# Optimization experiments

Measured on AMD Instinct MI355X. Metric: run time of the kernel, lower is better.

## Reference

```python
import jax, jax.numpy as jnp
import numpy as np

EMBED_DIM = 512
NUM_HEADS = 16
WINDOW = 8
SHIFT = 4
NUM_PATCHES = 64
NEG_INF = -1e9


def _attention_mask():
    # group map over the full patch grid, as in calculate_attention_mask
    P, s, ws = NUM_PATCHES, SHIFT, WINDOW
    g = np.zeros((P, P), dtype=np.float32)
    g[:, -s:] = 1
    g[-s:, :] = 2
    g[-s:, -s:] = 3
    nw = P // ws
    # (h ws a, w ws b) -> (h*w, ws*ws)
    gw = g.reshape(nw, ws, nw, ws).transpose(0, 2, 1, 3).reshape(nw * nw, ws * ws)
    same = gw[:, None, :] == gw[:, :, None]  # column - row == 0 -> allowed
    return jnp.asarray(same)  # (nW, S, S) bool, True = keep


def setup_inputs() -> dict:
    key = jax.random.key(0)
    ks = jax.random.split(key, 5)
    B, P, C = 16, NUM_PATCHES, EMBED_DIM
    sd = 1.0 / np.sqrt(C)
    return {
        "x": jax.random.normal(ks[0], (B, P, P, C), dtype=jnp.float32),
        "w_qkv": jax.random.normal(ks[1], (3 * C, C), dtype=jnp.float32) * sd,
        "b_qkv": jax.random.normal(ks[2], (3 * C,), dtype=jnp.float32) * 0.02,
        "w_out": jax.random.normal(ks[3], (C, C), dtype=jnp.float32) * sd,
        "b_out": jax.random.normal(ks[4], (C,), dtype=jnp.float32) * 0.02,
    }


def reference(x, w_qkv, b_qkv, w_out, b_out):
    B, P, _, C = x.shape
    ws, H = WINDOW, NUM_HEADS
    d = C // H
    nw = P // ws
    S = ws * ws
    scale = d ** (-0.5)

    # shift (roll backwards)
    xs = jnp.roll(x, (-SHIFT, -SHIFT), axis=(1, 2))
    # window partition: (B, nw, ws, nw, ws, C) -> (B*nw*nw, S, C)
    xw = xs.reshape(B, nw, ws, nw, ws, C).transpose(0, 1, 3, 2, 4, 5)
    xw = xw.reshape(B * nw * nw, S, C)

    qkv = xw @ w_qkv.T + b_qkv  # (Bn, S, 3C)
    q, k, v = jnp.split(qkv, 3, axis=-1)
    # head partition: (Bn, S, H, d) -> (Bn, H, S, d)
    part = lambda t: t.reshape(-1, S, H, d).transpose(0, 2, 1, 3)
    q, k, v = part(q), part(k), part(v)

    scores = jnp.einsum('bhqd,bhkd->bhqk', q, k) * scale  # (Bn, H, S, S)

    mask = _attention_mask()  # (nW, S, S) bool
    scores = scores.reshape(B, nw * nw, H, S, S)
    scores = jnp.where(mask[None, :, None], scores, NEG_INF)
    attn = jax.nn.softmax(scores, axis=-1)  # dropout p=0 (inference)
    attn = attn.reshape(B * nw * nw, H, S, S)

    out = jnp.einsum('bhqk,bhkd->bhqd', attn, v)  # (Bn, H, S, d)
    out = out.transpose(0, 2, 1, 3).reshape(B * nw * nw, S, C)  # merge heads
    out = out @ w_out.T + b_out

    # window merge: (B*nw*nw, S, C) -> (B, P, P, C)
    out = out.reshape(B, nw, nw, ws, ws, C).transpose(0, 1, 3, 2, 4, 5)
    out = out.reshape(B, P, P, C)
    # roll forwards
    return jnp.roll(out, (SHIFT, SHIFT), axis=(1, 2))
```

## Files before the change

### kernel.cpp

```cpp
#include <hip/hip_runtime.h>


using f16   = _Float16;
using f16x8 = __attribute__((ext_vector_type(8))) _Float16;
using f16x4 = __attribute__((ext_vector_type(4))) _Float16;
using f32x4 = __attribute__((ext_vector_type(4))) float;

#define MFMA16(a, b, c) __builtin_amdgcn_mfma_f32_16x16x32_f16((a), (b), (c), 0, 0, 0)
#define SCHEDBAR() __builtin_amdgcn_sched_barrier(0)
#define VMCNT0() asm volatile("s_waitcnt vmcnt(0)" ::: "memory")
#define LGKM0()  asm volatile("s_waitcnt lgkmcnt(0)" ::: "memory")
#define BAR()    __builtin_amdgcn_s_barrier()

static constexpr int QK_HALF = 65536 * 512;

__device__ __forceinline__ void nts4f(f32x4 v, float* p) {
  __builtin_nontemporal_store(v, (f32x4*)p);
}

__device__ __forceinline__ int tok2patch(int t) {
  int b = t >> 12, rem = t & 4095;
  int widx = rem >> 6, s = rem & 63;
  int pr = (((widx >> 3) << 3) + (s >> 3) + 4) & 63;
  int pc = (((widx & 7) << 3) + (s & 7) + 4) & 63;
  return ((b << 12) | (pr << 6) | pc) << 9;
}

__device__ __forceinline__ f16x8 cvt8(float4 a, float4 b) {
  f16x8 h = { (f16)a.x, (f16)a.y, (f16)a.z, (f16)a.w,
              (f16)b.x, (f16)b.y, (f16)b.z, (f16)b.w };
  return h;
}

__global__ __launch_bounds__(512, 2) void k_qkv(const float* __restrict__ x,
                                                const float* __restrict__ wq,
                                                const float* __restrict__ bq,
                                                f16* __restrict__ qk,
                                                f16* __restrict__ vt) {
  __shared__ __align__(16) char smem[86016];
  f16* const B0 = (f16*)smem;
  f16* const B1 = (f16*)(smem + 8192);

  const int tid = threadIdx.x;
  const int lane = tid & 63, wave = tid >> 6;
  const int jlo = lane & 15, g = lane >> 4;
  const int bm = blockIdx.x;

  const int nl = tid >> 2, kq = tid & 3;
  const int bslot = (kq ^ ((nl >> 1) & 3)) * 8;

  const int r0 = tok2patch(bm * 256 + wave * 32 + jlo);
  const int r1 = tok2patch(bm * 256 + wave * 32 + 16 + jlo);
  f16x8 af[2][16];
#pragma unroll
  for (int kg = 0; kg < 4; ++kg) {
    float4 t0[4][2], t1[4][2];
#pragma unroll
    for (int k4 = 0; k4 < 4; ++k4) {
      const int ko = (kg * 4 + k4) * 32 + g * 8;
      t0[k4][0] = *(const float4*)(x + r0 + ko);
      t0[k4][1] = *(const float4*)(x + r0 + ko + 4);
      t1[k4][0] = *(const float4*)(x + r1 + ko);
      t1[k4][1] = *(const float4*)(x + r1 + ko + 4);
    }
#pragma unroll
    for (int k4 = 0; k4 < 4; ++k4) {
      af[0][kg * 4 + k4] = cvt8(t0[k4][0], t0[k4][1]);
      af[1][kg * 4 + k4] = cvt8(t1[k4][0], t1[k4][1]);
    }
    SCHEDBAR();
  }

  f32x4 acc[2][8] = {};
  float4 rb[2];
#define LOADB(U2)                                                         \
  do {                                                                    \
    const int bn2_ = (U2) >> 4, k2_ = ((U2) & 15) * 32;                   \
    const float* bs_ = wq + (bn2_ * 128 + nl) * 512 + k2_ + kq * 8;       \
    rb[0] = *(const float4*)(bs_); rb[1] = *(const float4*)(bs_ + 4);     \
  } while (0)
#define WRITEB(Bp) do { *(f16x8*)((Bp) + nl * 32 + bslot) = cvt8(rb[0], rb[1]); } while (0)

  LOADB(0);
  SCHEDBAR();
  VMCNT0();
  WRITEB(B0);
  LOADB(1);
  LGKM0();
  BAR();

#pragma unroll 1
  for (int bn = 0; bn < 12; ++bn) {
    f16* const Cw = (f16*)(smem + 16384 + wave * 8704);
#pragma unroll
    for (int ks = 0; ks < 16; ++ks) {
      const int u = bn * 16 + ks;
      f16* const Bc = (u & 1) ? B1 : B0;
      f16* const Bn = (u & 1) ? B0 : B1;
      f16x8 bf[8];
#pragma unroll
      for (int nt = 0; nt < 8; ++nt) {
        const int n = nt * 16 + jlo;
        bf[nt] = *(const f16x8*)(Bc + n * 32 + ((g ^ ((n >> 1) & 3)) * 8));
      }
      __builtin_amdgcn_s_setprio(1);
#pragma unroll
      for (int mt = 0; mt < 2; ++mt)
#pragma unroll
        for (int nt = 0; nt < 8; ++nt)
          acc[mt][nt] = MFMA16(af[mt][ks], bf[nt], acc[mt][nt]);
      __builtin_amdgcn_s_setprio(0);
      VMCNT0();
      if (u + 1 < 192) WRITEB(Bn);
      SCHEDBAR();
      if (u + 2 < 192) LOADB(u + 2);
      LGKM0();
      BAR();
    }
    float bias[8];
#pragma unroll
    for (int nt = 0; nt < 8; ++nt) bias[nt] = bq[bn * 128 + nt * 16 + jlo];
    if (bn < 8) {
#pragma unroll
      for (int mt = 0; mt < 2; ++mt)
#pragma unroll
        for (int nt = 0; nt < 8; ++nt)
#pragma unroll
          for (int r = 0; r < 4; ++r)
            Cw[(mt * 16 + g * 4 + r) * 136 + nt * 16 + jlo] =
                (f16)(acc[mt][nt][r] + bias[nt]);
      LGKM0();
      f16* const gb = (bn < 4) ? (qk + bn * 128) : (qk + QK_HALF + (bn - 4) * 128);
#pragma unroll
      for (int p = 0; p < 8; ++p) {
        const int lr = (p >> 1) * 8 + (lane >> 3);
        const int ch = (p & 1) * 8 + (lane & 7);
        const int trow = bm * 256 + wave * 32 + lr;
        *(f16x8*)(gb + trow * 512 + ch * 8) = *(const f16x8*)(Cw + lr * 136 + ch * 8);
      }
    } else {
      const int w = (bm * 256 + wave * 32) >> 6;
      const int s0 = (wave * 32) & 63;
#pragma unroll
      for (int hf = 0; hf < 2; ++hf) {
#pragma unroll
        for (int n2 = 0; n2 < 4; ++n2) {
          const int nt = hf * 4 + n2;
#pragma unroll
          for (int mt = 0; mt < 2; ++mt) {
            f16x4 pk = { (f16)(acc[mt][nt][0] + bias[nt]), (f16)(acc[mt][nt][1] + bias[nt]),
                         (f16)(acc[mt][nt][2] + bias[nt]), (f16)(acc[mt][nt][3] + bias[nt]) };
            *(f16x4*)(Cw + (n2 * 16 + jlo) * 48 + mt * 16 + g * 4) = pk;
          }
        }
        LGKM0();
#pragma unroll
        for (int p = 0; p < 4; ++p) {
          const int cl = p * 16 + (lane >> 2);
          const int ch = lane & 3;
          const int n = (bn - 8) * 128 + hf * 64 + cl;
          const int h = n >> 5, d = n & 31;
          *(f16x8*)(vt + ((w * 16 + h) * 32 + d) * 64 + s0 + ch * 8) =
              *(const f16x8*)(Cw + cl * 48 + ch * 8);
        }
      }
    }
#pragma unroll
    for (int mt = 0; mt < 2; ++mt)
#pragma unroll
      for (int nt = 0; nt < 8; ++nt)
        acc[mt][nt] = (f32x4){0.f, 0.f, 0.f, 0.f};
  }
#undef LOADB
#undef WRITEB
}

__global__ __launch_bounds__(256) void k_attn(const f16* __restrict__ qk,
                                              const f16* __restrict__ vt,
                                              f16* __restrict__ ao) {
  __shared__ f16 P[4][64 * 72];
  const int w = blockIdx.x;
  const int widx = w & 63;
  const bool er = (widx >> 3) == 7;
  const bool ec = (widx & 7) == 7;
  const int tid = threadIdx.x;
  const int lane = tid & 63, wave = tid >> 6;
  const int jlo = lane & 15, g = lane >> 4;
  const int tb = w * 64;
  f16* Pw = P[wave];
  const float scale = 0.17677669529663687f;

#pragma unroll 1
  for (int hh = 0; hh < 4; ++hh) {
    const int h = wave * 4 + hh;
    f16x8 qa[4], kb[4];
#pragma unroll
    for (int mt = 0; mt < 4; ++mt)
      qa[mt] = *(const f16x8*)(qk + (tb + mt * 16 + jlo) * 512 + h * 32 + g * 8);
#pragma unroll
    for (int nt = 0; nt < 4; ++nt)
      kb[nt] = *(const f16x8*)(qk + QK_HALF + (tb + nt * 16 + jlo) * 512 + h * 32 + g * 8);
    f32x4 sc[4][4] = {};
#pragma unroll
    for (int mt = 0; mt < 4; ++mt)
#pragma unroll
      for (int nt = 0; nt < 4; ++nt)
        sc[mt][nt] = MFMA16(qa[mt], kb[nt], sc[mt][nt]);

    int gj[4];
#pragma unroll
    for (int nt = 0; nt < 4; ++nt) {
      int j = nt * 16 + jlo;
      gj[nt] = ((er && ((j >> 3) >= 4)) ? 2 : 0) | ((ec && ((j & 7) >= 4)) ? 1 : 0);
    }
    float rinv[4][4];
#pragma unroll
    for (int mt = 0; mt < 4; ++mt) {
#pragma unroll
      for (int r = 0; r < 4; ++r) {
        const int i = mt * 16 + g * 4 + r;
        const int gi = ((er && ((i >> 3) >= 4)) ? 2 : 0) | ((ec && ((i & 7) >= 4)) ? 1 : 0);
        float v0 = (gi == gj[0]) ? sc[mt][0][r] * scale : -1e9f;
        float v1 = (gi == gj[1]) ? sc[mt][1][r] * scale : -1e9f;
        float v2 = (gi == gj[2]) ? sc[mt][2][r] * scale : -1e9f;
        float v3 = (gi == gj[3]) ? sc[mt][3][r] * scale : -1e9f;
        float m = fmaxf(fmaxf(v0, v1), fmaxf(v2, v3));
        m = fmaxf(m, __shfl_xor(m, 1));
        m = fmaxf(m, __shfl_xor(m, 2));
        m = fmaxf(m, __shfl_xor(m, 4));
        m = fmaxf(m, __shfl_xor(m, 8));
        float p0 = __expf(v0 - m), p1 = __expf(v1 - m);
        float p2 = __expf(v2 - m), p3 = __expf(v3 - m);
        float s = p0 + p1 + p2 + p3;
        s += __shfl_xor(s, 1);
        s += __shfl_xor(s, 2);
        s += __shfl_xor(s, 4);
        s += __shfl_xor(s, 8);
        rinv[mt][r] = 1.0f / s;
        sc[mt][0][r] = p0; sc[mt][1][r] = p1; sc[mt][2][r] = p2; sc[mt][3][r] = p3;
      }
    }
#pragma unroll
    for (int mt = 0; mt < 4; ++mt)
#pragma unroll
      for (int nt = 0; nt < 4; ++nt)
#pragma unroll
        for (int r = 0; r < 4; ++r)
          Pw[(mt * 16 + g * 4 + r) * 72 + nt * 16 + jlo] = (f16)sc[mt][nt][r];
    asm volatile("s_waitcnt lgkmcnt(0)" ::: "memory");

    f32x4 o[4][2] = {};
#pragma unroll
    for (int ks = 0; ks < 2; ++ks) {
      f16x8 pa[4], vb[2];
#pragma unroll
      for (int mt = 0; mt < 4; ++mt)
        pa[mt] = *(const f16x8*)((const char*)Pw + (mt * 16 + jlo) * 144 + ks * 64 + g * 16);
#pragma unroll
      for (int nt = 0; nt < 2; ++nt)
        vb[nt] = *(const f16x8*)(vt + ((w * 16 + h) * 32 + nt * 16 + jlo) * 64 + ks * 32 + g * 8);
#pragma unroll
      for (int mt = 0; mt < 4; ++mt)
#pragma unroll
        for (int nt = 0; nt < 2; ++nt)
          o[mt][nt] = MFMA16(pa[mt], vb[nt], o[mt][nt]);
    }
#pragma unroll
    for (int mt = 0; mt < 4; ++mt)
#pragma unroll
      for (int nt = 0; nt < 2; ++nt)
#pragma unroll
        for (int r = 0; r < 4; ++r)
          Pw[(mt * 16 + g * 4 + r) * 40 + nt * 16 + jlo] =
              (f16)(o[mt][nt][r] * rinv[mt][r]);
    f16* arow = ao + (tb + lane) * 512 + h * 32;
#pragma unroll
    for (int c = 0; c < 4; ++c)
      *(f16x8*)(arow + c * 8) = *(const f16x8*)(Pw + lane * 40 + c * 8);
  }
}

__global__ __launch_bounds__(512, 2) void k_out(const f16* __restrict__ ao,
                                                const float* __restrict__ wo,
                                                const float* __restrict__ bo,
                                                float* __restrict__ out) {
  __shared__ __align__(16) char smem[86016];
  f16* const B0 = (f16*)smem;
  f16* const B1 = (f16*)(smem + 8192);

  const int tid = threadIdx.x;
  const int lane = tid & 63, wave = tid >> 6;
  const int jlo = lane & 15, g = lane >> 4;
  const int bm = blockIdx.x;

  const int nl = tid >> 2, kq = tid & 3;
  const int bslot = (kq ^ ((nl >> 1) & 3)) * 8;

  const f16* const a0 = ao + (bm * 256 + wave * 32 + jlo) * 512 + g * 8;
  const f16* const a1 = a0 + 16 * 512;
  f16x8 af[2][16];
#pragma unroll
  for (int ks = 0; ks < 16; ++ks) {
    af[0][ks] = *(const f16x8*)(a0 + ks * 32);
    af[1][ks] = *(const f16x8*)(a1 + ks * 32);
  }

  f32x4 acc[2][8] = {};
  float4 rb[2];
#define LOADB(U2)                                                         \
  do {                                                                    \
    const int bn2_ = (U2) >> 4, k2_ = ((U2) & 15) * 32;                   \
    const float* bs_ = wo + (bn2_ * 128 + nl) * 512 + k2_ + kq * 8;       \
    rb[0] = *(const float4*)(bs_); rb[1] = *(const float4*)(bs_ + 4);     \
  } while (0)
#define WRITEB(Bp) do { *(f16x8*)((Bp) + nl * 32 + bslot) = cvt8(rb[0], rb[1]); } while (0)

  LOADB(0);
  SCHEDBAR();
  VMCNT0();
  WRITEB(B0);
  LOADB(1);
  LGKM0();
  BAR();

#pragma unroll 1
  for (int bn = 0; bn < 4; ++bn) {
    float* const Cw = (float*)(smem + 16384 + wave * 8704);
#pragma unroll
    for (int ks = 0; ks < 16; ++ks) {
      const int u = bn * 16 + ks;
      f16* const Bc = (u & 1) ? B1 : B0;
      f16* const Bn = (u & 1) ? B0 : B1;
      f16x8 bf[8];
#pragma unroll
      for (int nt = 0; nt < 8; ++nt) {
        const int n = nt * 16 + jlo;
        bf[nt] = *(const f16x8*)(Bc + n * 32 + ((g ^ ((n >> 1) & 3)) * 8));
      }
      __builtin_amdgcn_s_setprio(1);
#pragma unroll
      for (int mt = 0; mt < 2; ++mt)
#pragma unroll
        for (int nt = 0; nt < 8; ++nt)
          acc[mt][nt] = MFMA16(af[mt][ks], bf[nt], acc[mt][nt]);
      __builtin_amdgcn_s_setprio(0);
      VMCNT0();
      if (u + 1 < 64) WRITEB(Bn);
      SCHEDBAR();
      if (u + 2 < 64) LOADB(u + 2);
      LGKM0();
      BAR();
    }
#pragma unroll
    for (int hf = 0; hf < 2; ++hf) {
#pragma unroll
      for (int n2 = 0; n2 < 4; ++n2) {
        const int nt = hf * 4 + n2;
        const float bias = bo[bn * 128 + nt * 16 + jlo];
#pragma unroll
        for (int mt = 0; mt < 2; ++mt)
#pragma unroll
          for (int r = 0; r < 4; ++r)
            Cw[(mt * 16 + g * 4 + r) * 68 + n2 * 16 + jlo] = acc[mt][nt][r] + bias;
      }
      LGKM0();
#pragma unroll
      for (int p = 0; p < 8; ++p) {
        const int lr = (p >> 1) * 8 + (lane >> 3);
        const int ch = (p & 1) * 8 + (lane & 7);
        const int trow = bm * 256 + wave * 32 + lr;
        nts4f(*(const f32x4*)(Cw + lr * 68 + ch * 4),
              out + tok2patch(trow) + bn * 128 + hf * 64 + ch * 4);
      }
      LGKM0();
    }
#pragma unroll
    for (int mt = 0; mt < 2; ++mt)
#pragma unroll
      for (int nt = 0; nt < 8; ++nt)
        acc[mt][nt] = (f32x4){0.f, 0.f, 0.f, 0.f};
  }
#undef LOADB
#undef WRITEB
}

extern "C" void kernel_launch(void* const* d_in, const int* in_sizes, int n_in,
                              void* d_out, int out_size, void* d_ws, size_t ws_size,
                              hipStream_t stream) {
  const float* x  = (const float*)d_in[0];
  const float* wq = (const float*)d_in[1];
  const float* bq = (const float*)d_in[2];
  const float* wo = (const float*)d_in[3];
  const float* bo = (const float*)d_in[4];
  float* out = (float*)d_out;

  f16* qk = (f16*)d_out;
  f16* ao = (f16*)d_ws;
  f16* vt = (f16*)((char*)d_ws + (64u << 20));

  k_qkv<<<dim3(256), 512, 0, stream>>>(x, wq, bq, qk, vt);
  k_attn<<<dim3(1024), 256, 0, stream>>>(qk, vt, ao);
  k_out<<<dim3(256), 512, 0, stream>>>(ao, wo, bo, out);
}
```

Measured before the change: 377.4 us.

## Process two k-steps per barrier with quad-buffered weight tiles in GEMM kernels

In both the QKV and output-projection GEMM kernels, the main loop now consumes two 32-wide k-slices per iteration, using four LDS B buffers and two register staging sets. This halves the number of block barriers and LDS-wait points per tile. The epilogue is folded into the flattened loop, and its scratch area moves to make room for the extra buffers. The trade-off is a larger LDS footprint and a runtime k-index into the A-fragment register array, which may force dynamic register indexing or scratch spills.

Result: slower. 420.7 us (+11.4%).

```diff
diff --git a/kernel.cpp b/kernel.cpp
--- a/kernel.cpp
+++ b/kernel.cpp
@@ -37,17 +37,16 @@
                                                 const float* __restrict__ bq,
                                                 f16* __restrict__ qk,
                                                 f16* __restrict__ vt) {
-  __shared__ __align__(16) char smem[86016];
-  f16* const B0 = (f16*)smem;
-  f16* const B1 = (f16*)(smem + 8192);
+  __shared__ __align__(16) char smem[102400];
+  f16* const B00 = (f16*)smem;
+  f16* const B01 = (f16*)(smem + 8192);
+  f16* const B10 = (f16*)(smem + 16384);
+  f16* const B11 = (f16*)(smem + 24576);
 
   const int tid = threadIdx.x;
   const int lane = tid & 63, wave = tid >> 6;
   const int jlo = lane & 15, g = lane >> 4;
   const int bm = blockIdx.x;
-
-  const int nl = tid >> 2, kq = tid & 3;
-  const int bslot = (kq ^ ((nl >> 1) & 3)) * 8;
 
   const int r0 = tok2patch(bm * 256 + wave * 32 + jlo);
   const int r1 = tok2patch(bm * 256 + wave * 32 + 16 + jlo);
@@ -71,32 +70,43 @@
     SCHEDBAR();
   }
 
+  const int nl = tid >> 2, kq = tid & 3;
+  const int bslot = (kq ^ ((nl >> 1) & 3)) * 8;
   f32x4 acc[2][8] = {};
-  float4 rb[2];
-#define LOADB(U2)                                                         \
+  float4 rbA[2], rbB[2];
+
+#define LOADB(U2, RB)                                                     \
   do {                                                                    \
     const int bn2_ = (U2) >> 4, k2_ = ((U2) & 15) * 32;                   \
     const float* bs_ = wq + (bn2_ * 128 + nl) * 512 + k2_ + kq * 8;       \
-    rb[0] = *(const float4*)(bs_); rb[1] = *(const float4*)(bs_ + 4);     \
+    RB[0] = *(const float4*)(bs_); RB[1] = *(const float4*)(bs_ + 4);     \
   } while (0)
-#define WRITEB(Bp) do { *(f16x8*)((Bp) + nl * 32 + bslot) = cvt8(rb[0], rb[1]); } while (0)
-
-  LOADB(0);
+#define WRITEB(Bp, RB) \
+  do { *(f16x8*)((Bp) + nl * 32 + bslot) = cvt8(RB[0], RB[1]); } while (0)
+
+  LOADB(0, rbA);
+  LOADB(1, rbB);
   SCHEDBAR();
   VMCNT0();
-  WRITEB(B0);
-  LOADB(1);
+  WRITEB(B00, rbA);
+  WRITEB(B01, rbB);
+  LOADB(2, rbA);
+  LOADB(3, rbB);
+  SCHEDBAR();
   LGKM0();
   BAR();
 
 #pragma unroll 1
-  for (int bn = 0; bn < 12; ++bn) {
-    f16* const Cw = (f16*)(smem + 16384 + wave * 8704);
-#pragma unroll
-    for (int ks = 0; ks < 16; ++ks) {
-      const int u = bn * 16 + ks;
-      f16* const Bc = (u & 1) ? B1 : B0;
-      f16* const Bn = (u & 1) ? B0 : B1;
+  for (int p = 0; p < 96; ++p) {
+    f16* const Bc0 = (p & 1) ? B10 : B00;
+    f16* const Bc1 = (p & 1) ? B11 : B01;
+    f16* const Bn0 = (p & 1) ? B00 : B10;
+    f16* const Bn1 = (p & 1) ? B01 : B11;
+
+#pragma unroll
+    for (int s2 = 0; s2 < 2; ++s2) {
+      const int kst = (2 * p + s2) & 15;
+      f16* const Bc = s2 ? Bc1 : Bc0;
       f16x8 bf[8];
 #pragma unroll
       for (int nt = 0; nt < 8; ++nt) {
@@ -108,68 +118,82 @@
       for (int mt = 0; mt < 2; ++mt)
 #pragma unroll
         for (int nt = 0; nt < 8; ++nt)
-          acc[mt][nt] = MFMA16(af[mt][ks], bf[nt], acc[mt][nt]);
+          acc[mt][nt] = MFMA16(af[mt][kst], bf[nt], acc[mt][nt]);
       __builtin_amdgcn_s_setprio(0);
+    }
+
+    if (p + 1 < 96) {
       VMCNT0();
-      if (u + 1 < 192) WRITEB(Bn);
+      WRITEB(Bn0, rbA);
+      WRITEB(Bn1, rbB);
       SCHEDBAR();
-      if (u + 2 < 192) LOADB(u + 2);
-      LGKM0();
-      BAR();
-    }
-    float bias[8];
-#pragma unroll
-    for (int nt = 0; nt < 8; ++nt) bias[nt] = bq[bn * 128 + nt * 16 + jlo];
-    if (bn < 8) {
-#pragma unroll
-      for (int mt = 0; mt < 2; ++mt)
-#pragma unroll
-        for (int nt = 0; nt < 8; ++nt)
-#pragma unroll
-          for (int r = 0; r < 4; ++r)
-            Cw[(mt * 16 + g * 4 + r) * 136 + nt * 16 + jlo] =
-                (f16)(acc[mt][nt][r] + bias[nt]);
-      LGKM0();
-      f16* const gb = (bn < 4) ? (qk + bn * 128) : (qk + QK_HALF + (bn - 4) * 128);
-#pragma unroll
-      for (int p = 0; p < 8; ++p) {
-        const int lr = (p >> 1) * 8 + (lane >> 3);
-        const int ch = (p & 1) * 8 + (lane & 7);
-        const int trow = bm * 256 + wave * 32 + lr;
-        *(f16x8*)(gb + trow * 512 + ch * 8) = *(const f16x8*)(Cw + lr * 136 + ch * 8);
-      }
-    } else {
-      const int w = (bm * 256 + wave * 32) >> 6;
-      const int s0 = (wave * 32) & 63;
-#pragma unroll
-      for (int hf = 0; hf < 2; ++hf) {
-#pragma unroll
-        for (int n2 = 0; n2 < 4; ++n2) {
-          const int nt = hf * 4 + n2;
-#pragma unroll
-          for (int mt = 0; mt < 2; ++mt) {
-            f16x4 pk = { (f16)(acc[mt][nt][0] + bias[nt]), (f16)(acc[mt][nt][1] + bias[nt]),
-                         (f16)(acc[mt][nt][2] + bias[nt]), (f16)(acc[mt][nt][3] + bias[nt]) };
-            *(f16x4*)(Cw + (n2 * 16 + jlo) * 48 + mt * 16 + g * 4) = pk;
-          }
+      if (2 * p + 4 < 192) LOADB(2 * p + 4, rbA);
+      if (2 * p + 5 < 192) LOADB(2 * p + 5, rbB);
+      SCHEDBAR();
+    }
+    LGKM0();
+    BAR();
+
+    if ((p & 7) == 7) {
+      const int bn = p >> 3;
+      float bias[8];
+#pragma unroll
+      for (int nt = 0; nt < 8; ++nt) bias[nt] = bq[bn * 128 + nt * 16 + jlo];
+      if (bn < 8) {
+        f16* const Cw = (f16*)(smem + 32768 + wave * 8704);
+#pragma unroll
+        for (int mt = 0; mt < 2; ++mt)
+#pragma unroll
+          for (int nt = 0; nt < 8; ++nt)
+#pragma unroll
+            for (int r = 0; r < 4; ++r)
+              Cw[(mt * 16 + g * 4 + r) * 136 + nt * 16 + jlo] =
+                  (f16)(acc[mt][nt][r] + bias[nt]);
+        LGKM0();
+        f16* const gb = (bn < 4) ? (qk + bn * 128) : (qk + QK_HALF + (bn - 4) * 128);
+#pragma unroll
+        for (int q = 0; q < 8; ++q) {
+          const int lr = (q >> 1) * 8 + (lane >> 3);
+          const int ch = (q & 1) * 8 + (lane & 7);
+          const int trow = bm * 256 + wave * 32 + lr;
+          *(f16x8*)(gb + trow * 512 + ch * 8) = *(const f16x8*)(Cw + lr * 136 + ch * 8);
         }
         LGKM0();
-#pragma unroll
-        for (int p = 0; p < 4; ++p) {
-          const int cl = p * 16 + (lane >> 2);
-          const int ch = lane & 3;
-          const int n = (bn - 8) * 128 + hf * 64 + cl;
-          const int h = n >> 5, d = n & 31;
-          *(f16x8*)(vt + ((w * 16 + h) * 32 + d) * 64 + s0 + ch * 8) =
-              *(const f16x8*)(Cw + cl * 48 + ch * 8);
+      } else {
+        f16* const Cw = (f16*)(smem + 32768 + wave * 8704);
+        const int w = bm * 4 + (wave >> 1);
+        const int s0 = (wave * 32) & 63;
+#pragma unroll
+        for (int hf = 0; hf < 2; ++hf) {
+#pragma unroll
+          for (int n2 = 0; n2 < 4; ++n2) {
+            const int nt = hf * 4 + n2;
+#pragma unroll
+            for (int mt = 0; mt < 2; ++mt) {
+              f16x4 pk = { (f16)(acc[mt][nt][0] + bias[nt]), (f16)(acc[mt][nt][1] + bias[nt]),
+                           (f16)(acc[mt][nt][2] + bias[nt]), (f16)(acc[mt][nt][3] + bias[nt]) };
+              *(f16x4*)(Cw + (n2 * 16 + jlo) * 48 + mt * 16 + g * 4) = pk;
+            }
+          }
+          LGKM0();
+#pragma unroll
+          for (int q = 0; q < 4; ++q) {
+            const int cl = q * 16 + (lane >> 2);
+            const int ch = lane & 3;
+            const int n = (bn - 8) * 128 + hf * 64 + cl;
+            const int h = n >> 5, d = n & 31;
+            *(f16x8*)(vt + ((w * 16 + h) * 32 + d) * 64 + s0 + ch * 8) =
+                *(const f16x8*)(Cw + cl * 48 + ch * 8);
+          }
+          LGKM0();
         }
       }
-    }
-#pragma unroll
-    for (int mt = 0; mt < 2; ++mt)
-#pragma unroll
-      for (int nt = 0; nt < 8; ++nt)
-        acc[mt][nt] = (f32x4){0.f, 0.f, 0.f, 0.f};
+#pragma unroll
+      for (int mt = 0; mt < 2; ++mt)
+#pragma unroll
+        for (int nt = 0; nt < 8; ++nt)
+          acc[mt][nt] = (f32x4){0.f, 0.f, 0.f, 0.f};
+    }
   }
 #undef LOADB
 #undef WRITEB
@@ -284,18 +308,17 @@
                                                 const float* __restrict__ wo,
                                                 const float* __restrict__ bo,
                                                 float* __restrict__ out) {
-  __shared__ __align__(16) char smem[86016];
-  f16* const B0 = (f16*)smem;
-  f16* const B1 = (f16*)(smem + 8192);
+  __shared__ __align__(16) char smem[102400];
+  f16* const B00 = (f16*)smem;
+  f16* const B01 = (f16*)(smem + 8192);
+  f16* const B10 = (f16*)(smem + 16384);
+  f16* const B11 = (f16*)(smem + 24576);
 
   const int tid = threadIdx.x;
   const int lane = tid & 63, wave = tid >> 6;
   const int jlo = lane & 15, g = lane >> 4;
   const int bm = blockIdx.x;
 
-  const int nl = tid >> 2, kq = tid & 3;
-  const int bslot = (kq ^ ((nl >> 1) & 3)) * 8;
-
   const f16* const a0 = ao + (bm * 256 + wave * 32 + jlo) * 512 + g * 8;
   const f16* const a1 = a0 + 16 * 512;
   f16x8 af[2][16];
@@ -305,32 +328,43 @@
     af[1][ks] = *(const f16x8*)(a1 + ks * 32);
   }
 
+  const int nl = tid >> 2, kq = tid & 3;
+  const int bslot = (kq ^ ((nl >> 1) & 3)) * 8;
   f32x4 acc[2][8] = {};
-  float4 rb[2];
-#define LOADB(U2)                                                         \
+  float4 rbA[2], rbB[2];
+
+#define LOADB(U2, RB)                                                     \
   do {                                                                    \
     const int bn2_ = (U2) >> 4, k2_ = ((U2) & 15) * 32;                   \
     const float* bs_ = wo + (bn2_ * 128 + nl) * 512 + k2_ + kq * 8;       \
-    rb[0] = *(const float4*)(bs_); rb[1] = *(const float4*)(bs_ + 4);     \
+    RB[0] = *(const float4*)(bs_); RB[1] = *(const float4*)(bs_ + 4);     \
   } while (0)
-#define WRITEB(Bp) do { *(f16x8*)((Bp) + nl * 32 + bslot) = cvt8(rb[0], rb[1]); } while (0)
-
-  LOADB(0);
+#define WRITEB(Bp, RB) \
+  do { *(f16x8*)((Bp) + nl * 32 + bslot) = cvt8(RB[0], RB[1]); } while (0)
+
+  LOADB(0, rbA);
+  LOADB(1, rbB);
   SCHEDBAR();
   VMCNT0();
-  WRITEB(B0);
-  LOADB(1);
+  WRITEB(B00, rbA);
+  WRITEB(B01, rbB);
+  LOADB(2, rbA);
+  LOADB(3, rbB);
+  SCHEDBAR();
   LGKM0();
   BAR();
 
 #pragma unroll 1
-  for (int bn = 0; bn < 4; ++bn) {
-    float* const Cw = (float*)(smem + 16384 + wave * 8704);
-#pragma unroll
-    for (int ks = 0; ks < 16; ++ks) {
-      const int u = bn * 16 + ks;
-      f16* const Bc = (u & 1) ? B1 : B0;
-      f16* const Bn = (u & 1) ? B0 : B1;
+  for (int p = 0; p < 32; ++p) {
+    f16* const Bc0 = (p & 1) ? B10 : B00;
+    f16* const Bc1 = (p & 1) ? B11 : B01;
+    f16* const Bn0 = (p & 1) ? B00 : B10;
+    f16* const Bn1 = (p & 1) ? B01 : B11;
+
+#pragma unroll
+    for (int s2 = 0; s2 < 2; ++s2) {
+      const int kst = (2 * p + s2) & 15;
+      f16* const Bc = s2 ? Bc1 : Bc0;
       f16x8 bf[8];
 #pragma unroll
       for (int nt = 0; nt < 8; ++nt) {
@@ -342,43 +376,54 @@
       for (int mt = 0; mt < 2; ++mt)
 #pragma unroll
         for (int nt = 0; nt < 8; ++nt)
-          acc[mt][nt] = MFMA16(af[mt][ks], bf[nt], acc[mt][nt]);
+          acc[mt][nt] = MFMA16(af[mt][kst], bf[nt], acc[mt][nt]);
       __builtin_amdgcn_s_setprio(0);
+    }
+
+    if (p + 1 < 32) {
       VMCNT0();
-      if (u + 1 < 64) WRITEB(Bn);
+      WRITEB(Bn0, rbA);
+      WRITEB(Bn1, rbB);
       SCHEDBAR();
-      if (u + 2 < 64) LOADB(u + 2);
-      LGKM0();
-      BAR();
-    }
-#pragma unroll
-    for (int hf = 0; hf < 2; ++hf) {
-#pragma unroll
-      for (int n2 = 0; n2 < 4; ++n2) {
-        const int nt = hf * 4 + n2;
-        const float bias = bo[bn * 128 + nt * 16 + jlo];
-#pragma unroll
-        for (int mt = 0; mt < 2; ++mt)
-#pragma unroll
-          for (int r = 0; r < 4; ++r)
-            Cw[(mt * 16 + g * 4 + r) * 68 + n2 * 16 + jlo] = acc[mt][nt][r] + bias;
+      if (2 * p + 4 < 64) LOADB(2 * p + 4, rbA);
+      if (2 * p + 5 < 64) LOADB(2 * p + 5, rbB);
+      SCHEDBAR();
+    }
+    LGKM0();
+    BAR();
+
+    if ((p & 7) == 7) {
+      const int bn = p >> 3;
+      float* const Cw = (float*)(smem + 32768 + wave * 8704);
+#pragma unroll
+      for (int hf = 0; hf < 2; ++hf) {
+#pragma unroll
+        for (int n2 = 0; n2 < 4; ++n2) {
+          const int nt = hf * 4 + n2;
+          const float bias = bo[bn * 128 + nt * 16 + jlo];
+#pragma unroll
+          for (int mt = 0; mt < 2; ++mt)
+#pragma unroll
+            for (int r = 0; r < 4; ++r)
+              Cw[(mt * 16 + g * 4 + r) * 68 + n2 * 16 + jlo] = acc[mt][nt][r] + bias;
+        }
+        LGKM0();
+#pragma unroll
+        for (int q = 0; q < 8; ++q) {
+          const int lr = (q >> 1) * 8 + (lane >> 3);
+          const int ch = (q & 1) * 8 + (lane & 7);
+          const int trow = bm * 256 + wave * 32 + lr;
+          nts4f(*(const f32x4*)(Cw + lr * 68 + ch * 4),
+                out + tok2patch(trow) + bn * 128 + hf * 64 + ch * 4);
+        }
+        LGKM0();
       }
-      LGKM0();
-#pragma unroll
-      for (int p = 0; p < 8; ++p) {
-        const int lr = (p >> 1) * 8 + (lane >> 3);
-        const int ch = (p & 1) * 8 + (lane & 7);
-        const int trow = bm * 256 + wave * 32 + lr;
-        nts4f(*(const f32x4*)(Cw + lr * 68 + ch * 4),
-              out + tok2patch(trow) + bn * 128 + hf * 64 + ch * 4);
-      }
-      LGKM0();
-    }
-#pragma unroll
-    for (int mt = 0; mt < 2; ++mt)
-#pragma unroll
-      for (int nt = 0; nt < 8; ++nt)
-        acc[mt][nt] = (f32x4){0.f, 0.f, 0.f, 0.f};
+#pragma unroll
+      for (int mt = 0; mt < 2; ++mt)
+#pragma unroll
+        for (int nt = 0; nt < 8; ++nt)
+          acc[mt][nt] = (f32x4){0.f, 0.f, 0.f, 0.f};
+    }
   }
 #undef LOADB
 #undef WRITEB
```

## Split QKV GEMM N-dimension across two blocks per M tile for more occupancy

Applied to the files above, without the earlier changes.

The QKV projection grid doubles from 256 to 512 blocks, with each block computing half of the 12 output column tiles (6 tiles) for a 256-token M tile. Shared memory per block shrinks (the C staging buffer is now written in two 64-column halves) and launch bounds request 4 blocks per CU. This aims to fill all CUs, since 256 blocks underfill a 256-CU part, at the cost of each block reloading and converting its x rows, which doubles the x reads. Register pressure under the tighter launch bound could cause spills.

Result: slower. 467.7 us (+23.9%).

```diff
diff --git a/kernel.cpp b/kernel.cpp
--- a/kernel.cpp
+++ b/kernel.cpp
@@ -32,22 +32,21 @@
   return h;
 }
 
-__global__ __launch_bounds__(512, 2) void k_qkv(const float* __restrict__ x,
+__global__ __launch_bounds__(512, 4) void k_qkv(const float* __restrict__ x,
                                                 const float* __restrict__ wq,
                                                 const float* __restrict__ bq,
                                                 f16* __restrict__ qk,
                                                 f16* __restrict__ vt) {
-  __shared__ __align__(16) char smem[86016];
+  __shared__ __align__(16) char smem[65536];
   f16* const B0 = (f16*)smem;
   f16* const B1 = (f16*)(smem + 8192);
 
   const int tid = threadIdx.x;
   const int lane = tid & 63, wave = tid >> 6;
   const int jlo = lane & 15, g = lane >> 4;
-  const int bm = blockIdx.x;
-
-  const int nl = tid >> 2, kq = tid & 3;
-  const int bslot = (kq ^ ((nl >> 1) & 3)) * 8;
+  const int blk = blockIdx.x;
+  const int bm = blk >> 1;
+  const int bnbase = (blk & 1) * 6;
 
   const int r0 = tok2patch(bm * 256 + wave * 32 + jlo);
   const int r1 = tok2patch(bm * 256 + wave * 32 + 16 + jlo);
@@ -71,11 +70,13 @@
     SCHEDBAR();
   }
 
+  const int nl = tid >> 2, kq = tid & 3;
+  const int bslot = (kq ^ ((nl >> 1) & 3)) * 8;
   f32x4 acc[2][8] = {};
   float4 rb[2];
 #define LOADB(U2)                                                         \
   do {                                                                    \
-    const int bn2_ = (U2) >> 4, k2_ = ((U2) & 15) * 32;                   \
+    const int bn2_ = bnbase + ((U2) >> 4), k2_ = ((U2) & 15) * 32;        \
     const float* bs_ = wq + (bn2_ * 128 + nl) * 512 + k2_ + kq * 8;       \
     rb[0] = *(const float4*)(bs_); rb[1] = *(const float4*)(bs_ + 4);     \
   } while (0)
@@ -90,11 +91,10 @@
   BAR();
 
 #pragma unroll 1
-  for (int bn = 0; bn < 12; ++bn) {
-    f16* const Cw = (f16*)(smem + 16384 + wave * 8704);
+  for (int bt = 0; bt < 6; ++bt) {
 #pragma unroll
     for (int ks = 0; ks < 16; ++ks) {
-      const int u = bn * 16 + ks;
+      const int u = bt * 16 + ks;
       f16* const Bc = (u & 1) ? B1 : B0;
       f16* const Bn = (u & 1) ? B0 : B1;
       f16x8 bf[8];
@@ -111,35 +111,45 @@
           acc[mt][nt] = MFMA16(af[mt][ks], bf[nt], acc[mt][nt]);
       __builtin_amdgcn_s_setprio(0);
       VMCNT0();
-      if (u + 1 < 192) WRITEB(Bn);
+      if (u + 1 < 96) WRITEB(Bn);
       SCHEDBAR();
-      if (u + 2 < 192) LOADB(u + 2);
+      if (u + 2 < 96) LOADB(u + 2);
       LGKM0();
       BAR();
     }
+    const int bn = bnbase + bt;
     float bias[8];
 #pragma unroll
     for (int nt = 0; nt < 8; ++nt) bias[nt] = bq[bn * 128 + nt * 16 + jlo];
     if (bn < 8) {
-#pragma unroll
-      for (int mt = 0; mt < 2; ++mt)
-#pragma unroll
-        for (int nt = 0; nt < 8; ++nt)
-#pragma unroll
-          for (int r = 0; r < 4; ++r)
-            Cw[(mt * 16 + g * 4 + r) * 136 + nt * 16 + jlo] =
-                (f16)(acc[mt][nt][r] + bias[nt]);
-      LGKM0();
+      f16* const Cw = (f16*)(smem + 16384 + wave * 6144);
       f16* const gb = (bn < 4) ? (qk + bn * 128) : (qk + QK_HALF + (bn - 4) * 128);
 #pragma unroll
-      for (int p = 0; p < 8; ++p) {
-        const int lr = (p >> 1) * 8 + (lane >> 3);
-        const int ch = (p & 1) * 8 + (lane & 7);
-        const int trow = bm * 256 + wave * 32 + lr;
-        *(f16x8*)(gb + trow * 512 + ch * 8) = *(const f16x8*)(Cw + lr * 136 + ch * 8);
+      for (int hf = 0; hf < 2; ++hf) {
+#pragma unroll
+        for (int n2 = 0; n2 < 4; ++n2) {
+          const int nt = hf * 4 + n2;
+#pragma unroll
+          for (int mt = 0; mt < 2; ++mt)
+#pragma unroll
+            for (int r = 0; r < 4; ++r)
+              Cw[(mt * 16 + g * 4 + r) * 72 + n2 * 16 + jlo] =
+                  (f16)(acc[mt][nt][r] + bias[nt]);
+        }
+        LGKM0();
+#pragma unroll
+        for (int q = 0; q < 4; ++q) {
+          const int lr = q * 8 + (lane >> 3);
+          const int ch = lane & 7;
+          const int trow = bm * 256 + wave * 32 + lr;
+          *(f16x8*)(gb + trow * 512 + hf * 64 + ch * 8) =
+              *(const f16x8*)(Cw + lr * 72 + ch * 8);
+        }
+        LGKM0();
       }
     } else {
-      const int w = (bm * 256 + wave * 32) >> 6;
+      f16* const Cw = (f16*)(smem + 16384 + wave * 6144);
+      const int w = bm * 4 + (wave >> 1);
       const int s0 = (wave * 32) & 63;
 #pragma unroll
       for (int hf = 0; hf < 2; ++hf) {
@@ -155,14 +165,15 @@
         }
         LGKM0();
 #pragma unroll
-        for (int p = 0; p < 4; ++p) {
-          const int cl = p * 16 + (lane >> 2);
+        for (int q = 0; q < 4; ++q) {
+          const int cl = q * 16 + (lane >> 2);
           const int ch = lane & 3;
           const int n = (bn - 8) * 128 + hf * 64 + cl;
           const int h = n >> 5, d = n & 31;
           *(f16x8*)(vt + ((w * 16 + h) * 32 + d) * 64 + s0 + ch * 8) =
               *(const f16x8*)(Cw + cl * 48 + ch * 8);
         }
+        LGKM0();
       }
     }
 #pragma unroll
@@ -365,9 +376,9 @@
       }
       LGKM0();
 #pragma unroll
-      for (int p = 0; p < 8; ++p) {
-        const int lr = (p >> 1) * 8 + (lane >> 3);
-        const int ch = (p & 1) * 8 + (lane & 7);
+      for (int q = 0; q < 8; ++q) {
+        const int lr = (q >> 1) * 8 + (lane >> 3);
+        const int ch = (q & 1) * 8 + (lane & 7);
         const int trow = bm * 256 + wave * 32 + lr;
         nts4f(*(const f32x4*)(Cw + lr * 68 + ch * 4),
               out + tok2patch(trow) + bn * 128 + hf * 64 + ch * 4);
@@ -398,7 +409,7 @@
   f16* ao = (f16*)d_ws;
   f16* vt = (f16*)((char*)d_ws + (64u << 20));
 
-  k_qkv<<<dim3(256), 512, 0, stream>>>(x, wq, bq, qk, vt);
+  k_qkv<<<dim3(512), 512, 0, stream>>>(x, wq, bq, qk, vt);
   k_attn<<<dim3(1024), 256, 0, stream>>>(qk, vt, ao);
   k_out<<<dim3(256), 512, 0, stream>>>(ao, wo, bo, out);
 }
```
